# Optimization experiments

Measured on AMD Instinct MI355X. Metric: run time of the kernel, lower is better.

## Reference

```python
import jax, jax.numpy as jnp
import numpy as np

B, S, C = 32, 512, 384
MAX_LEN = 4096
MAX_DUR = 16


def setup_inputs() -> dict:
    key = jax.random.key(0)
    kx, kd = jax.random.split(key)
    x = jax.random.normal(kx, (B, S, C), dtype=jnp.float32)
    durations = jax.random.randint(kd, (B, S), 0, MAX_DUR, dtype=jnp.int32)
    return {"x": x, "durations": durations, "max_length": MAX_LEN}


def reference(x, durations, max_length):
    # Round (no-op for int durations, kept for faithfulness to torch.round().long())
    d = jnp.round(durations.astype(jnp.float32)).astype(jnp.int32)  # [B, S]
    # _limit_durations is equivalent to clipping the cumulative sum at max_length:
    # the first token crossing max_length gets truncated, all later tokens zeroed.
    ends = jnp.clip(jnp.cumsum(d, axis=1), 0, max_length)          # [B, S]
    total = ends[:, -1]                                            # [B]
    t = jnp.arange(max_length, dtype=jnp.int32)                    # [T]
    # frame t belongs to phoneme j where starts[j] <= t < ends[j];
    # searchsorted(ends, t, 'right') skips zero-duration tokens automatically.
    idx = jax.vmap(lambda e: jnp.searchsorted(e, t, side='right'))(ends)  # [B, T]
    mel_masks = t[None, :] >= total[:, None]                       # [B, T] True = pad
    idx_c = jnp.clip(idx, 0, x.shape[1] - 1)
    expanded = jnp.take_along_axis(x, idx_c[:, :, None], axis=1)   # [B, T, C]
    expanded = jnp.where(mel_masks[:, :, None], jnp.zeros((), x.dtype), expanded)
    return expanded, mel_masks
```

## Files before the change

kernel.cpp:

```cpp
#include <hip/hip_runtime.h>

#define BATCH 32
#define SEQ 512
#define CH4 96
#define MAXL 4096
#define THREADS 256
#define SLABS 64
#define ROWS_PB 64
#define ITERS 24

typedef float v4f __attribute__((ext_vector_type(4)));
typedef int   v4i __attribute__((ext_vector_type(4)));

__global__ __launch_bounds__(THREADS) void lr_gather(
    const v4f* __restrict__ x,
    const v4i* __restrict__ dur4,
    const int* __restrict__ max_len_p,
    v4f* __restrict__ out,
    float* __restrict__ out_mask)
{
    __shared__ int s_end[SEQ];
    __shared__ int s_src[ROWS_PB];

    const int tid  = threadIdx.x;
    const int bid  = blockIdx.x;
    const int b    = bid >> 6;
    const int slab = bid & (SLABS - 1);
    const int r0   = slab * ROWS_PB;

    if (tid < 64) {
        const v4i* dp = dur4 + b * (SEQ / 4) + tid * 2;
        v4i d0 = dp[0], d1 = dp[1];
        int lane_sum = d0.x + d0.y + d0.z + d0.w + d1.x + d1.y + d1.z + d1.w;
        int incl = lane_sum;
        #pragma unroll
        for (int off = 1; off < 64; off <<= 1) {
            int v = __shfl_up(incl, off, 64);
            if (tid >= off) incl += v;
        }
        int cum = incl - lane_sum;
        const int maxlen = max_len_p[0];
        const int base = tid * 8;
        cum += d0.x; s_end[base + 0] = min(cum, maxlen);
        cum += d0.y; s_end[base + 1] = min(cum, maxlen);
        cum += d0.z; s_end[base + 2] = min(cum, maxlen);
        cum += d0.w; s_end[base + 3] = min(cum, maxlen);
        cum += d1.x; s_end[base + 4] = min(cum, maxlen);
        cum += d1.y; s_end[base + 5] = min(cum, maxlen);
        cum += d1.z; s_end[base + 6] = min(cum, maxlen);
        cum += d1.w; s_end[base + 7] = min(cum, maxlen);
    }
    __syncthreads();

    const int total = s_end[SEQ - 1];

    if (tid < ROWS_PB) {
        const int t = r0 + tid;
        int lo = 0, hi = SEQ;
        #pragma unroll
        for (int s = 0; s < 10; ++s) {
            int mid = (lo + hi) >> 1;
            mid = min(mid, SEQ - 1);
            const bool le = (s_end[mid] <= t);
            lo = le ? mid + 1 : lo;
            hi = le ? hi : mid;
        }
        s_src[tid] = (t < total) ? lo : -1;
        out_mask[(b << 12) + t] = (t >= total) ? 1.0f : 0.0f;
    }
    __syncthreads();

    const v4f* xb = x + (size_t)b * (SEQ * CH4);
    v4f* ob = out + ((size_t)(b << 12) + r0) * CH4;
    const v4f vzero = (v4f){0.f, 0.f, 0.f, 0.f};

    #pragma unroll 6
    for (int it = 0; it < ITERS; ++it) {
        const int g = it * THREADS + tid;
        const int r = g / CH4;
        const int c = g - r * CH4;
        const int j = s_src[r];
        v4f v = vzero;
        if (j >= 0) v = xb[j * CH4 + c];
        ob[g] = v;
    }
}

extern "C" void kernel_launch(void* const* d_in, const int* in_sizes, int n_in,
                              void* d_out, int out_size, void* d_ws, size_t ws_size,
                              hipStream_t stream) {
    const v4f* x = (const v4f*)d_in[0];
    const v4i* dur4 = (const v4i*)d_in[1];
    const int* max_len_p = (const int*)d_in[2];
    float* out = (float*)d_out;
    float* out_mask = out + (size_t)BATCH * MAXL * CH4 * 4;

    lr_gather<<<BATCH * SLABS, THREADS, 0, stream>>>(
        x, dur4, max_len_p, (v4f*)out, out_mask);
}
```

Baseline: 231.3 us.

## Split index computation into separate kernel and use nontemporal stores for output

Moves the per-batch duration prefix sum and binary search into a small first kernel that writes indices into the mask region of the output. The gather kernel then reads those indices, converts them in place to mask floats, and expands rows. Previously every one of the 64 slab blocks per batch redid the full 512-entry scan, and that redundant work is now removed. Output stores become nontemporal to avoid polluting the cache, at the cost of an extra kernel launch and an aliasing read-then-write of the mask buffer.

```diff
diff --git a/kernel.cpp b/kernel.cpp
--- a/kernel.cpp
+++ b/kernel.cpp
@@ -12,21 +12,15 @@
 typedef float v4f __attribute__((ext_vector_type(4)));
 typedef int   v4i __attribute__((ext_vector_type(4)));
 
-__global__ __launch_bounds__(THREADS) void lr_gather(
-    const v4f* __restrict__ x,
+__global__ __launch_bounds__(THREADS) void lr_index(
     const v4i* __restrict__ dur4,
     const int* __restrict__ max_len_p,
-    v4f* __restrict__ out,
-    float* __restrict__ out_mask)
+    int* __restrict__ idxbuf)
 {
     __shared__ int s_end[SEQ];
-    __shared__ int s_src[ROWS_PB];
-
     const int tid  = threadIdx.x;
-    const int bid  = blockIdx.x;
-    const int b    = bid >> 6;
-    const int slab = bid & (SLABS - 1);
-    const int r0   = slab * ROWS_PB;
+    const int b    = blockIdx.x >> 3;
+    const int part = blockIdx.x & 7;
 
     if (tid < 64) {
         const v4i* dp = dur4 + b * (SEQ / 4) + tid * 2;
@@ -53,9 +47,11 @@
     __syncthreads();
 
     const int total = s_end[SEQ - 1];
+    const int t0 = (part << 9) + tid;
 
-    if (tid < ROWS_PB) {
-        const int t = r0 + tid;
+    #pragma unroll
+    for (int k = 0; k < 2; ++k) {
+        const int t = t0 + (k << 8);
         int lo = 0, hi = SEQ;
         #pragma unroll
         for (int s = 0; s < 10; ++s) {
@@ -65,8 +61,28 @@
             lo = le ? mid + 1 : lo;
             hi = le ? hi : mid;
         }
-        s_src[tid] = (t < total) ? lo : -1;
-        out_mask[(b << 12) + t] = (t >= total) ? 1.0f : 0.0f;
+        idxbuf[(b << 12) + t] = (t < total) ? lo : -1;
+    }
+}
+
+__global__ __launch_bounds__(THREADS) void lr_expand(
+    const v4f* __restrict__ x,
+    const int* idxbuf,
+    float* out_mask,
+    v4f* __restrict__ out)
+{
+    __shared__ int s_src[ROWS_PB];
+    const int tid  = threadIdx.x;
+    const int bid  = blockIdx.x;
+    const int b    = bid >> 6;
+    const int slab = bid & (SLABS - 1);
+    const int r0   = slab * ROWS_PB;
+
+    int myidx = 0;
+    if (tid < ROWS_PB) {
+        myidx = idxbuf[(b << 12) + r0 + tid];
+        s_src[tid] = myidx;
+        out_mask[(b << 12) + r0 + tid] = (myidx < 0) ? 1.0f : 0.0f;
     }
     __syncthreads();
 
@@ -82,7 +98,7 @@
         const int j = s_src[r];
         v4f v = vzero;
         if (j >= 0) v = xb[j * CH4 + c];
-        ob[g] = v;
+        __builtin_nontemporal_store(v, &ob[g]);
     }
 }
 
@@ -95,6 +111,8 @@
     float* out = (float*)d_out;
     float* out_mask = out + (size_t)BATCH * MAXL * CH4 * 4;
 
-    lr_gather<<<BATCH * SLABS, THREADS, 0, stream>>>(
-        x, dur4, max_len_p, (v4f*)out, out_mask);
+    lr_index<<<BATCH * 8, THREADS, 0, stream>>>(
+        dur4, max_len_p, (int*)out_mask);
+    lr_expand<<<BATCH * SLABS, THREADS, 0, stream>>>(
+        x, (const int*)out_mask, out_mask, (v4f*)out);
 }
```

New measurement: 243.2 us. 1.05x slower.
